# Kernel tuning notes

Hardware: AMD Instinct MI355X
Metric: run time of the kernel (lower is better)

The kernel has to match this reference:

```python
import jax, jax.numpy as jnp
import numpy as np

N = 10000      # nodes
E = 160000     # edges (before self-loops)
IN = 256
NEG_SLOPE = 0.2  # PyG GATConv default


def gat_layer(x, src, dst, W, a_src, a_dst, bias, heads, concat, n):
    # x: [n, in_dim]; W: [in_dim, heads*C]; a_src/a_dst: [heads, C]
    C = W.shape[1] // heads
    h = (x @ W).reshape(n, heads, C)                      # [n,H,C]
    es = jnp.einsum('nhc,hc->nh', h, a_src)               # [n,H]
    ed = jnp.einsum('nhc,hc->nh', h, a_dst)               # [n,H]
    e = jax.nn.leaky_relu(es[src] + ed[dst], NEG_SLOPE)   # [E,H]
    # segment softmax over destination node (every node has a self-loop)
    emax = jax.ops.segment_max(e, dst, num_segments=n)    # [n,H]
    al = jnp.exp(e - emax[dst])                           # [E,H]
    den = jax.ops.segment_sum(al, dst, num_segments=n)    # [n,H]
    al = al / den[dst]
    out = jax.ops.segment_sum(h[src] * al[:, :, None], dst, num_segments=n)  # [n,H,C]
    out = out.reshape(n, heads * C) if concat else out.mean(axis=1)
    return out + bias


def setup_inputs() -> dict:
    key = jax.random.key(0)
    ks = jax.random.split(key, 16)
    s = 0.05
    p = lambda k, shp: jax.random.normal(k, shp, dtype=jnp.float32) * s
    return {
        'x': jax.random.normal(ks[0], (N, IN), dtype=jnp.float32),
        'edge_index': jax.random.randint(ks[1], (2, E), 0, N, dtype=jnp.int64),
        'proj_w': p(ks[2], (IN, 512)), 'proj_b': jnp.zeros((512,), jnp.float32),
        'w1': p(ks[3], (512, 4 * 512)),  'as1': p(ks[4], (4, 512)), 'ad1': p(ks[5], (4, 512)),  'b1': jnp.zeros((2048,), jnp.float32),
        'w2': p(ks[6], (2048, 4 * 512)), 'as2': p(ks[7], (4, 512)), 'ad2': p(ks[8], (4, 512)),  'b2': jnp.zeros((2048,), jnp.float32),
        'w3': p(ks[9], (2048, 2 * 512)), 'as3': p(ks[10], (2, 512)), 'ad3': p(ks[11], (2, 512)), 'b3': jnp.zeros((512,), jnp.float32),
    }


def reference(x, edge_index, proj_w, proj_b, w1, as1, ad1, b1,
              w2, as2, ad2, b2, w3, as3, ad3, b3):
    n = x.shape[0]
    loops = jnp.arange(n, dtype=edge_index.dtype)
    src = jnp.concatenate([edge_index[0], loops])   # PyG add_self_loops=True
    dst = jnp.concatenate([edge_index[1], loops])
    h = x @ proj_w + proj_b                         # dropout is identity in eval
    h = gat_layer(h, src, dst, w1, as1, ad1, b1, 4, True, n)
    h = jax.nn.elu(h)
    h = gat_layer(h, src, dst, w2, as2, ad2, b2, 4, True, n)
    h = jax.nn.elu(h)
    h = gat_layer(h, src, dst, w3, as3, ad3, b3, 2, False, n)
    return h
```

## Files before the change

### kernel.cpp

```cpp
#include <hip/hip_runtime.h>
#include <hip/hip_bf16.h>
#include <math.h>

#define CDIV(a,b) (((a)+(b)-1)/(b))

typedef __bf16  bf16x8 __attribute__((ext_vector_type(8)));
typedef float   f32x4  __attribute__((ext_vector_type(4)));
typedef unsigned short u16x8 __attribute__((ext_vector_type(8)));
typedef unsigned short u16x4 __attribute__((ext_vector_type(4)));

__device__ __forceinline__ float bf2f(unsigned short u) {
    union { unsigned int i; float f; } x; x.i = ((unsigned int)u) << 16; return x.f;
}
__device__ __forceinline__ unsigned short f2bf(float f) {
    union { float f; unsigned int i; } x; x.f = f;
    unsigned int r = x.i + 0x7fff + ((x.i >> 16) & 1);
    return (unsigned short)(r >> 16);
}

__global__ void hist_kernel(const int* __restrict__ ei, int* __restrict__ deg,
                            int E, int Et) {
    int e = blockIdx.x * blockDim.x + threadIdx.x;
    if (e >= Et) return;
    int d = (e < E) ? ei[E + e] : (e - E);
    atomicAdd(&deg[d], 1);
}

__global__ void scan_kernel(const int* __restrict__ deg, int* __restrict__ off, int n) {
    __shared__ int wsum[16];
    __shared__ int carry_s;
    int t = threadIdx.x, lane = t & 63, wv = t >> 6;
    if (t == 0) carry_s = 0;
    __syncthreads();
    for (int base = 0; base < n; base += 1024) {
        int v = (base + t < n) ? deg[base + t] : 0;
        int x = v;
#pragma unroll
        for (int o = 1; o < 64; o <<= 1) {
            int y = __shfl_up(x, o);
            if (lane >= o) x += y;
        }
        if (lane == 63) wsum[wv] = x;
        __syncthreads();
        if (wv == 0 && lane < 16) {
            int s = wsum[lane];
#pragma unroll
            for (int o = 1; o < 16; o <<= 1) {
                int y = __shfl_up(s, o);
                if (lane >= o) s += y;
            }
            wsum[lane] = s;
        }
        __syncthreads();
        int wprev = (wv == 0) ? 0 : wsum[wv - 1];
        int incl = carry_s + wprev + x;
        if (base + t < n) off[base + t] = incl - v;
        __syncthreads();
        if (t == 1023) carry_s = incl;
        __syncthreads();
    }
    if (t == 0) off[n] = carry_s;
}

__global__ void scatter_kernel(const int* __restrict__ ei, const int* __restrict__ off,
                               int* __restrict__ cur, int* __restrict__ csr,
                               int E, int Et) {
    int e = blockIdx.x * blockDim.x + threadIdx.x;
    if (e >= Et) return;
    int s, d;
    if (e < E) { s = ei[e]; d = ei[E + e]; } else { s = e - E; d = s; }
    int pos = off[d] + atomicAdd(&cur[d], 1);
    csr[pos] = s;
}

__global__ void prep_t_kernel(const float* __restrict__ wa, __hip_bfloat16* __restrict__ wta,
                              const float* __restrict__ wb, __hip_bfloat16* __restrict__ wtb,
                              const float* __restrict__ wc, __hip_bfloat16* __restrict__ wtc,
                              int t0, int t1, int t2) {
    __shared__ float tile[32][33];
    int bid = blockIdx.x;
    const float* w; __hip_bfloat16* wt; int K, N, r;
    if (bid < t0)      { w = wa; wt = wta; K = 512;  N = 2048; r = bid; }
    else if (bid < t1) { w = wb; wt = wtb; K = 2048; N = 2048; r = bid - t0; }
    else               { w = wc; wt = wtc; K = 2048; N = 1024; r = bid - t1; }
    (void)t2;
    int kt = K >> 5;
    int kb = (r % kt) * 32, nb = (r / kt) * 32;
    int tx = threadIdx.x & 31, ty = threadIdx.x >> 5;
    for (int i = ty; i < 32; i += 8)
        tile[i][tx] = w[(size_t)(kb + i) * N + nb + tx];
    __syncthreads();
    for (int i = ty; i < 32; i += 8)
        wt[(size_t)(nb + i) * K + kb + tx] = __float2bfloat16(tile[tx][i]);
}

__global__ void cvt2_kernel(const float* __restrict__ a, __hip_bfloat16* __restrict__ ao,
                            int na4,
                            const float* __restrict__ b, __hip_bfloat16* __restrict__ bo,
                            int nb4) {
    int i = blockIdx.x * blockDim.x + threadIdx.x;
    const float* src; __hip_bfloat16* dst; int idx;
    if (i < na4) { src = a; dst = ao; idx = i * 4; }
    else if (i < na4 + nb4) { src = b; dst = bo; idx = (i - na4) * 4; }
    else return;
    float4 v = *(const float4*)(src + idx);
    dst[idx + 0] = __float2bfloat16(v.x);
    dst[idx + 1] = __float2bfloat16(v.y);
    dst[idx + 2] = __float2bfloat16(v.z);
    dst[idx + 3] = __float2bfloat16(v.w);
}

__global__ void beff_kernel(const float* __restrict__ pb, const float* __restrict__ w1,
                            float* __restrict__ beff, int N) {
    int j  = blockIdx.x * 256 + threadIdx.x;
    int k0 = blockIdx.y * 64;
    float s = 0.f;
#pragma unroll
    for (int k = 0; k < 64; k++)
        s = fmaf(pb[k0 + k], w1[(size_t)(k0 + k) * N + j], s);
    atomicAdd(&beff[j], s);
}

__global__ void va_kernel(const __hip_bfloat16* __restrict__ w_efft,
                          const float* __restrict__ b_eff,
                          const float* __restrict__ as1, const float* __restrict__ ad1,
                          const float* __restrict__ b1,
                          float* __restrict__ va, float* __restrict__ cvec,
                          float* __restrict__ b1s) {
    int j = blockIdx.x, t = threadIdx.x;
    if (j == 8) {
        for (int i = t; i < 2048; i += 256) b1s[i] = b_eff[i] + b1[i];
        return;
    }
    int h = j & 3;
    const float* a = ((j < 4) ? as1 : ad1) + h * 512;
    __shared__ float aLDS[512];
    __shared__ float red[256];
    for (int c = t; c < 512; c += 256) aLDS[c] = a[c];
    __syncthreads();
    float acc = 0.f;
    const unsigned short* wb = (const unsigned short*)w_efft + (size_t)h * 512 * 256 + t;
    for (int c = 0; c < 512; c++)
        acc = fmaf(aLDS[c], bf2f(wb[(size_t)c * 256]), acc);
    va[j * 256 + t] = acc;
    float cp = b_eff[h * 512 + t] * aLDS[t] + b_eff[h * 512 + 256 + t] * aLDS[256 + t];
    red[t] = cp;
    __syncthreads();
    for (int s = 128; s > 0; s >>= 1) {
        if (t < s) red[t] += red[t + s];
        __syncthreads();
    }
    if (t == 0) cvec[j] = red[0];
}

__global__ void es1_kernel(const __hip_bfloat16* __restrict__ x_bf,
                           const float* __restrict__ va, const float* __restrict__ cvec,
                           float* __restrict__ es, float* __restrict__ ed) {
    int node = blockIdx.x, l = threadIdx.x;
    u16x4 xv = *(const u16x4*)((const unsigned short*)x_bf + (size_t)node * 256 + l * 4);
    float xf[4];
#pragma unroll
    for (int k = 0; k < 4; k++) xf[k] = bf2f(xv[k]);
    float dot[8];
#pragma unroll
    for (int j = 0; j < 8; j++) {
        float4 v = *(const float4*)(va + j * 256 + l * 4);
        dot[j] = xf[0] * v.x + xf[1] * v.y + xf[2] * v.z + xf[3] * v.w;
    }
#pragma unroll
    for (int j = 0; j < 8; j++)
        for (int o = 32; o; o >>= 1) dot[j] += __shfl_down(dot[j], o);
    if (l == 0) {
#pragma unroll
        for (int h = 0; h < 4; h++) {
            es[node * 4 + h] = dot[h] + cvec[h];
            ed[node * 4 + h] = dot[4 + h] + cvec[4 + h];
        }
    }
}

__global__ __launch_bounds__(256) void agg1x_kernel(
    const __hip_bfloat16* __restrict__ x_bf, const float* __restrict__ es,
    const float* __restrict__ ed, const int* __restrict__ csr,
    const int* __restrict__ off, __hip_bfloat16* __restrict__ z)
{
    __shared__ float alds[64][4];
    __shared__ int   slds[64];
    int d = blockIdx.x, t = threadIdx.x;
    int beg = off[d], end = off[d + 1];
    float acc[4] = {0.f, 0.f, 0.f, 0.f}, den[4] = {0.f, 0.f, 0.f, 0.f};
    float edd[4];
#pragma unroll
    for (int h = 0; h < 4; h++) edd[h] = ed[d * 4 + h];
    const unsigned short* xb = (const unsigned short*)x_bf;

    for (int cb = beg; cb < end; cb += 64) {
        int cl = end - cb; if (cl > 64) cl = 64;
        int i = t >> 2, h = t & 3;
        if (i < cl) {
            int s = csr[cb + i];
            if (h == 0) slds[i] = s;
            float e = es[s * 4 + h] + edd[h];
            e = (e > 0.f) ? e : 0.2f * e;
            alds[i][h] = __expf(e);
        }
        __syncthreads();
        for (int ii = 0; ii < cl; ii++) {
            int s = slds[ii];
            float xv = bf2f(xb[(size_t)s * 256 + t]);
#pragma unroll
            for (int hh = 0; hh < 4; hh++) {
                float a = alds[ii][hh];
                den[hh] += a;
                acc[hh] = fmaf(a, xv, acc[hh]);
            }
        }
        __syncthreads();
    }
    unsigned short* zb = (unsigned short*)z + (size_t)d * 1024;
#pragma unroll
    for (int h = 0; h < 4; h++)
        zb[h * 256 + t] = f2bf(acc[h] / den[h]);
}

__device__ __forceinline__ void gload16(void* lds, const void* g) {
    __builtin_amdgcn_global_load_lds(
        (const __attribute__((address_space(1))) void*)g,
        (__attribute__((address_space(3))) void*)lds, 16, 0, 0);
}

__global__ __launch_bounds__(256) void gemm_bf16_kernel(
    const __hip_bfloat16* __restrict__ A,
    const __hip_bfloat16* __restrict__ BT,
    const float* __restrict__ bias,
    __hip_bfloat16* __restrict__ Cb,
    int M, int N, int K, int lda, int hko, int do_elu,
    int MB, int NB, int XT, int NBH)
{
    __shared__ __align__(16) __hip_bfloat16 As[128 * 32];
    __shared__ __align__(16) __hip_bfloat16 Bs[128 * 32];

    const int bid  = blockIdx.x;
    const int xcd  = bid & 7;
    const int slot = bid >> 3;
    const int per_yh = XT * NBH;
    const int yh    = slot / per_yh;
    const int rem   = slot - yh * per_yh;
    const int x_sub = rem / NBH;
    const int ys    = rem - x_sub * NBH;
    const int yb    = yh * NBH + ys;
    const int xb    = xcd * XT + x_sub;
    if (xb >= MB || yb >= NB) return;

    const int tid = threadIdx.x;
    const int m0 = xb * 128, n0 = yb * 128;
    const int w = tid >> 6, l = tid & 63;
    const int wm = (w & 1) * 64, wn = (w >> 1) * 64;
    const int lm = l & 15, lq = l >> 4;

    f32x4 acc[4][4] = {};

    const int arow = tid >> 2;
    const int acol = (tid & 3) * 8;
    const __hip_bfloat16* Ag = A + (size_t)(m0 + arow) * lda + acol + (n0 >> 9) * hko;
    const __hip_bfloat16* Bg = BT + (size_t)(n0 + arow) * K + acol;
    char* AsW = (char*)As + (w << 10);
    char* BsW = (char*)Bs + (w << 10);

    for (int k0 = 0; k0 < K; k0 += 32) {
        gload16(AsW,        Ag + k0);
        gload16(AsW + 4096, Ag + (size_t)64 * lda + k0);
        gload16(BsW,        Bg + k0);
        gload16(BsW + 4096, Bg + (size_t)64 * K + k0);
        __syncthreads();
        bf16x8 af[4], bfr[4];
#pragma unroll
        for (int i = 0; i < 4; i++)
            af[i] = *(const bf16x8*)(As + (wm + i * 16 + lm) * 32 + lq * 8);
#pragma unroll
        for (int j = 0; j < 4; j++)
            bfr[j] = *(const bf16x8*)(Bs + (wn + j * 16 + lm) * 32 + lq * 8);
#pragma unroll
        for (int i = 0; i < 4; i++)
#pragma unroll
            for (int j = 0; j < 4; j++)
                acc[i][j] = __builtin_amdgcn_mfma_f32_16x16x32_bf16(
                    af[i], bfr[j], acc[i][j], 0, 0, 0);
        __syncthreads();
    }

#pragma unroll
    for (int i = 0; i < 4; i++) {
        int rb = m0 + wm + i * 16 + lq * 4;
#pragma unroll
        for (int r = 0; r < 4; r++) {
            int row = rb + r;
            if (row >= M) continue;
#pragma unroll
            for (int j = 0; j < 4; j++) {
                int col = n0 + wn + j * 16 + lm;
                float v = acc[i][j][r];
                if (bias) v += bias[col];
                if (do_elu) v = (v > 0.f) ? v : expm1f(v);
                Cb[(size_t)row * N + col] = __float2bfloat16(v);
            }
        }
    }
}

__global__ __launch_bounds__(512, 2) void gemm256_kernel(
    const __hip_bfloat16* __restrict__ A,
    const __hip_bfloat16* __restrict__ BT,
    __hip_bfloat16* __restrict__ Cb,
    int M, int N, int K, int MT, int nfull)
{
    __shared__ __align__(16) char smem[131072];
    const int NT = K >> 6;

    const int cpx  = gridDim.x >> 3;
    const int bid  = blockIdx.x;
    const int slot = (bid & 7) * cpx + (bid >> 3);
    int mt, ntl;
    if (slot < nfull) { mt = slot % MT; ntl = slot / MT; }
    else              { ntl = nfull / MT; mt = (nfull % MT) + (slot - nfull); }
    const int m0 = mt << 8, n0 = ntl << 8;

    const int tid = threadIdx.x;
    const int w  = tid >> 6, l = tid & 63;
    const int wr = w >> 2, wc = w & 3;
    const int lm = l & 15, lq = l >> 4;

    const int srow = tid >> 3;
    const int scol = ((l & 7) << 3) ^ ((l >> 3) << 3);
    const __hip_bfloat16* As0 = A  + (size_t)(m0 + srow) * K + scol;
    const __hip_bfloat16* Bs0 = BT + (size_t)(n0 + srow) * K + scol;
    const size_t rs64  = (size_t)64  * K;
    const size_t rs128 = (size_t)128 * K;
    char* const stA = smem +          ((size_t)w << 10);
    char* const stB = smem + 65536 +  ((size_t)w << 10);

    auto STAGE_A = [&](int par, int hf, int tt) {
        char* d = stA + (((par << 1) | hf) << 14);
        const __hip_bfloat16* s = As0 + (size_t)hf * rs128 + (tt << 6);
        gload16(d,        s);
        gload16(d + 8192, s + rs64);
    };
    auto STAGE_B = [&](int par, int hf, int tt) {
        char* d = stB + (((par << 1) | hf) << 14);
        const __hip_bfloat16* s = Bs0 + (size_t)hf * rs128 + (tt << 6);
        gload16(d,        s);
        gload16(d + 8192, s + rs64);
    };

    const int roff = lm << 7;
    const int xm   = (lm & 7) << 4;
    const int off0 = (lq << 4) ^ xm;
    const int off1 = off0 ^ 64;
    const int bsel = 65536 + ((wc & 1) << 13);

    f32x4  acc[8][4] = {};
    bf16x8 af[8][2];
    bf16x8 bfr[2][2];

    STAGE_A(0, 0, 0); STAGE_A(0, 1, 0);
    STAGE_B(0, 0, 0); STAGE_B(0, 1, 0);
    STAGE_A(1, 0, 1); STAGE_A(1, 1, 1);
    asm volatile("s_waitcnt vmcnt(4)" ::: "memory");
    __builtin_amdgcn_s_barrier();

    for (int t = 0; t < NT; ++t) {
        const int par = t & 1;
        const char* aS = smem + (((par << 1) | wr)        << 14) + roff;
        const char* bS = smem + (((par << 1) | (wc >> 1)) << 14) + bsel + roff;

#pragma unroll
        for (int i = 0; i < 4; ++i) {
            af[i][0] = *(const bf16x8*)(aS + i * 2048 + off0);
            af[i][1] = *(const bf16x8*)(aS + i * 2048 + off1);
        }
#pragma unroll
        for (int j = 0; j < 2; ++j) {
            bfr[j][0] = *(const bf16x8*)(bS + j * 2048 + off0);
            bfr[j][1] = *(const bf16x8*)(bS + j * 2048 + off1);
        }
        if (t + 1 < NT) STAGE_B(par ^ 1, 0, t + 1);
        __builtin_amdgcn_s_barrier();
        asm volatile("s_waitcnt lgkmcnt(0)" ::: "memory");
        __builtin_amdgcn_sched_barrier(0);
        __builtin_amdgcn_s_setprio(1);
#pragma unroll
        for (int i = 0; i < 4; ++i)
#pragma unroll
            for (int j = 0; j < 2; ++j) {
                acc[i][j] = __builtin_amdgcn_mfma_f32_16x16x32_bf16(af[i][0], bfr[j][0], acc[i][j], 0, 0, 0);
                acc[i][j] = __builtin_amdgcn_mfma_f32_16x16x32_bf16(af[i][1], bfr[j][1], acc[i][j], 0, 0, 0);
            }
        __builtin_amdgcn_s_setprio(0);
        __builtin_amdgcn_s_barrier();

#pragma unroll
        for (int i = 4; i < 8; ++i) {
            af[i][0] = *(const bf16x8*)(aS + i * 2048 + off0);
            af[i][1] = *(const bf16x8*)(aS + i * 2048 + off1);
        }
        if (t + 1 < NT) STAGE_B(par ^ 1, 1, t + 1);
        __builtin_amdgcn_s_barrier();
        asm volatile("s_waitcnt lgkmcnt(0)" ::: "memory");
        __builtin_amdgcn_sched_barrier(0);
        __builtin_amdgcn_s_setprio(1);
#pragma unroll
        for (int i = 4; i < 8; ++i)
#pragma unroll
            for (int j = 0; j < 2; ++j) {
                acc[i][j] = __builtin_amdgcn_mfma_f32_16x16x32_bf16(af[i][0], bfr[j][0], acc[i][j], 0, 0, 0);
                acc[i][j] = __builtin_amdgcn_mfma_f32_16x16x32_bf16(af[i][1], bfr[j][1], acc[i][j], 0, 0, 0);
            }
        __builtin_amdgcn_s_setprio(0);
        __builtin_amdgcn_s_barrier();

#pragma unroll
        for (int j = 0; j < 2; ++j) {
            bfr[j][0] = *(const bf16x8*)(bS + (j + 2) * 2048 + off0);
            bfr[j][1] = *(const bf16x8*)(bS + (j + 2) * 2048 + off1);
        }
        if (t + 2 < NT) STAGE_A(par, 0, t + 2);
        __builtin_amdgcn_s_barrier();
        asm volatile("s_waitcnt lgkmcnt(0)" ::: "memory");
        __builtin_amdgcn_sched_barrier(0);
        __builtin_amdgcn_s_setprio(1);
#pragma unroll
        for (int i = 0; i < 4; ++i)
#pragma unroll
            for (int j = 0; j < 2; ++j) {
                acc[i][j + 2] = __builtin_amdgcn_mfma_f32_16x16x32_bf16(af[i][0], bfr[j][0], acc[i][j + 2], 0, 0, 0);
                acc[i][j + 2] = __builtin_amdgcn_mfma_f32_16x16x32_bf16(af[i][1], bfr[j][1], acc[i][j + 2], 0, 0, 0);
            }
        __builtin_amdgcn_s_setprio(0);
        __builtin_amdgcn_s_barrier();

        if (t + 2 < NT) STAGE_A(par, 1, t + 2);
        __builtin_amdgcn_s_barrier();
        __builtin_amdgcn_sched_barrier(0);
        __builtin_amdgcn_s_setprio(1);
#pragma unroll
        for (int i = 4; i < 8; ++i)
#pragma unroll
            for (int j = 0; j < 2; ++j) {
                acc[i][j + 2] = __builtin_amdgcn_mfma_f32_16x16x32_bf16(af[i][0], bfr[j][0], acc[i][j + 2], 0, 0, 0);
                acc[i][j + 2] = __builtin_amdgcn_mfma_f32_16x16x32_bf16(af[i][1], bfr[j][1], acc[i][j + 2], 0, 0, 0);
            }
        __builtin_amdgcn_s_setprio(0);
        if (t + 2 < NT)      { asm volatile("s_waitcnt vmcnt(4)" ::: "memory"); }
        else if (t + 1 < NT) { asm volatile("s_waitcnt vmcnt(0)" ::: "memory"); }
        __builtin_amdgcn_s_barrier();
    }

#pragma unroll
    for (int i = 0; i < 8; ++i) {
        int rb = m0 + wr * 128 + i * 16 + lq * 4;
#pragma unroll
        for (int r = 0; r < 4; ++r) {
            int row = rb + r;
            if (row >= M) continue;
#pragma unroll
            for (int j = 0; j < 4; ++j) {
                int col = n0 + wc * 64 + j * 16 + lm;
                Cb[(size_t)row * N + col] = __float2bfloat16(acc[i][j][r]);
            }
        }
    }
}

__global__ __launch_bounds__(256, 2) void gemm128_kernel(
    const __hip_bfloat16* __restrict__ A,
    const __hip_bfloat16* __restrict__ BT,
    __hip_bfloat16* __restrict__ Cb,
    int M, int N, int K, int mode, int RT)
{
    __shared__ __align__(16) char smem[65536];
    const int NT = K >> 6;

    const int cpx  = gridDim.x >> 3;
    const int bid  = blockIdx.x;
    const int slot = (bid & 7) * cpx + (bid >> 3);
    int r, c;
    if (mode == 0) { r = slot % RT; c = slot / RT; }
    else {
        if (slot < 96) { c = 12 + slot / 48; r = 32 + slot % 48; }
        else           { int u = slot - 96; c = 14 + u / 80; r = u % 80; }
    }
    const int m0 = r << 7, n0 = c << 7;

    const int tid = threadIdx.x;
    const int w = tid >> 6, l = tid & 63;
    const int wm = (w & 1) << 6, wn = (w >> 1) << 6;
    const int lm = l & 15, lq = l >> 4;

    const int srow = tid >> 3;
    const int scol = (((tid & 7) ^ ((tid >> 3) & 7)) << 3);
    const __hip_bfloat16* Ag = A  + (size_t)(m0 + srow) * K + scol;
    const __hip_bfloat16* Bg = BT + (size_t)(n0 + srow) * K + scol;
    const size_t rs32 = (size_t)32 * K;
    char* const dA = smem +         ((size_t)w << 10);
    char* const dB = smem + 16384 + ((size_t)w << 10);

    auto STAGE = [&](int par, int tt) {
        char* pa = dA + (par << 15);
        char* pb = dB + (par << 15);
        const __hip_bfloat16* sa = Ag + (tt << 6);
        const __hip_bfloat16* sb = Bg + (tt << 6);
#pragma unroll
        for (int s = 0; s < 4; ++s) {
            gload16(pa + (s << 12), sa + (size_t)s * rs32);
            gload16(pb + (s << 12), sb + (size_t)s * rs32);
        }
    };

    const int roff = lm << 7;
    const int off0 = (lq << 4) ^ ((lm & 7) << 4);
    const int off1 = off0 ^ 64;

    f32x4 acc[4][4] = {};

    STAGE(0, 0);
    asm volatile("s_waitcnt vmcnt(0)" ::: "memory");
    __builtin_amdgcn_s_barrier();

    for (int t = 0; t < NT; ++t) {
        const int par = t & 1;
        if (t + 1 < NT) STAGE(par ^ 1, t + 1);
        const char* aS = smem + (par << 15) +         wm * 128 + roff;
        const char* bS = smem + (par << 15) + 16384 + wn * 128 + roff;
        bf16x8 af[4][2], bfr[4][2];
#pragma unroll
        for (int i = 0; i < 4; ++i) {
            af[i][0]  = *(const bf16x8*)(aS + i * 2048 + off0);
            af[i][1]  = *(const bf16x8*)(aS + i * 2048 + off1);
            bfr[i][0] = *(const bf16x8*)(bS + i * 2048 + off0);
            bfr[i][1] = *(const bf16x8*)(bS + i * 2048 + off1);
        }
        asm volatile("s_waitcnt lgkmcnt(0)" ::: "memory");
        __builtin_amdgcn_sched_barrier(0);
        __builtin_amdgcn_s_setprio(1);
#pragma unroll
        for (int i = 0; i < 4; ++i)
#pragma unroll
            for (int j = 0; j < 4; ++j) {
                acc[i][j] = __builtin_amdgcn_mfma_f32_16x16x32_bf16(af[i][0], bfr[j][0], acc[i][j], 0, 0, 0);
                acc[i][j] = __builtin_amdgcn_mfma_f32_16x16x32_bf16(af[i][1], bfr[j][1], acc[i][j], 0, 0, 0);
            }
        __builtin_amdgcn_s_setprio(0);
        if (t + 1 < NT) asm volatile("s_waitcnt vmcnt(0)" ::: "memory");
        __builtin_amdgcn_s_barrier();
    }

#pragma unroll
    for (int i = 0; i < 4; ++i) {
        int rb = m0 + wm + i * 16 + lq * 4;
#pragma unroll
        for (int r2 = 0; r2 < 4; ++r2) {
            int row = rb + r2;
            if (row >= M) continue;
#pragma unroll
            for (int j = 0; j < 4; ++j) {
                int col = n0 + wn + j * 16 + lm;
                Cb[(size_t)row * N + col] = __float2bfloat16(acc[i][j][r2]);
            }
        }
    }
}

__global__ void esed_kernel(const __hip_bfloat16* __restrict__ h,
                            const float* __restrict__ a_src,
                            const float* __restrict__ a_dst,
                            float* __restrict__ es, float* __restrict__ ed, int H) {
    int nidx = blockIdx.x;
    int t = threadIdx.x;
    int head = t >> 6, lane = t & 63;
    const unsigned short* hp =
        (const unsigned short*)h + (size_t)nidx * H * 512 + head * 512 + lane * 8;
    const float* sp = a_src + head * 512 + lane * 8;
    const float* dp = a_dst + head * 512 + lane * 8;
    u16x8 hv = *(const u16x8*)hp;
    float4 s0 = *(const float4*)sp, s1 = *(const float4*)(sp + 4);
    float4 d0 = *(const float4*)dp, d1 = *(const float4*)(dp + 4);
    float hf[8];
#pragma unroll
    for (int k = 0; k < 8; k++) hf[k] = bf2f(hv[k]);
    float s = hf[0]*s0.x + hf[1]*s0.y + hf[2]*s0.z + hf[3]*s0.w
            + hf[4]*s1.x + hf[5]*s1.y + hf[6]*s1.z + hf[7]*s1.w;
    float d = hf[0]*d0.x + hf[1]*d0.y + hf[2]*d0.z + hf[3]*d0.w
            + hf[4]*d1.x + hf[5]*d1.y + hf[6]*d1.z + hf[7]*d1.w;
    for (int o = 32; o; o >>= 1) { s += __shfl_down(s, o); d += __shfl_down(d, o); }
    if (lane == 0) { es[nidx * H + head] = s; ed[nidx * H + head] = d; }
}

template<int H, int SHIFT>
__global__ __launch_bounds__(256) void alpharec_kernel(
    const float* __restrict__ es, const float* __restrict__ ed,
    const int* __restrict__ csr, const int* __restrict__ off,
    uint2* __restrict__ rec, int n)
{
    int d = blockIdx.x * 4 + (threadIdx.x >> 6);
    if (d >= n) return;
    int lane = threadIdx.x & 63;
    int beg = off[d], end = off[d + 1];
    float edd[H], den[H];
#pragma unroll
    for (int h = 0; h < H; h++) { edd[h] = ed[d * H + h]; den[h] = 0.f; }
    for (int i = beg + lane; i < end; i += 64) {
        int s = csr[i];
#pragma unroll
        for (int h = 0; h < H; h++) {
            float e = es[s * H + h] + edd[h];
            e = (e > 0.f) ? e : 0.2f * e;
            den[h] += __expf(e);
        }
    }
#pragma unroll
    for (int h = 0; h < H; h++) {
        for (int o = 32; o; o >>= 1) den[h] += __shfl_down(den[h], o);
        den[h] = __shfl(den[h], 0);
        den[h] = 1.f / den[h];
    }
    for (int i = beg + lane; i < end; i += 64) {
        int s = csr[i];
        unsigned obytes = ((unsigned)s) << SHIFT;
#pragma unroll
        for (int h = 0; h < H; h++) {
            float e = es[s * H + h] + edd[h];
            e = (e > 0.f) ? e : 0.2f * e;
            float a = __expf(e) * den[h];
            rec[(size_t)i * H + h] = make_uint2(obytes, __float_as_uint(a));
        }
    }
}

__global__ __launch_bounds__(256) void agg2s_kernel(
    const __hip_bfloat16* __restrict__ h, const uint2* __restrict__ rec,
    const int* __restrict__ off, const float* __restrict__ bias,
    __hip_bfloat16* __restrict__ outB, int n)
{
    const int bid   = blockIdx.x;
    const int slice = bid & 7;
    const int head  = slice >> 1;
    const int wvs   = (bid >> 3) * 4 + (threadIdx.x >> 6);
    const int lane  = threadIdx.x & 63;
    const int half  = lane >> 5;
    const int c0    = slice * 256 + (lane & 31) * 8;
    const unsigned c0b = (unsigned)c0 * 2;
    const char* hb = (const char*)h;
    float bv[8];
#pragma unroll
    for (int k = 0; k < 8; k++) bv[k] = bias[c0 + k];

    for (int d = wvs; d < n; d += 1024) {
        int beg = off[d], end = off[d + 1];
        float acc[8] = {0.f, 0.f, 0.f, 0.f, 0.f, 0.f, 0.f, 0.f};
        int i = beg + half;
        for (; i + 2 < end; i += 4) {
            uint2 r0 = rec[i * 4 + head];
            uint2 r1 = rec[(i + 2) * 4 + head];
            u16x8 v0 = *(const u16x8*)(hb + (size_t)(r0.x + c0b));
            u16x8 v1 = *(const u16x8*)(hb + (size_t)(r1.x + c0b));
            float a0 = __uint_as_float(r0.y);
            float a1 = __uint_as_float(r1.y);
#pragma unroll
            for (int k = 0; k < 8; k++) acc[k] = fmaf(a0, bf2f(v0[k]), acc[k]);
#pragma unroll
            for (int k = 0; k < 8; k++) acc[k] = fmaf(a1, bf2f(v1[k]), acc[k]);
        }
        for (; i < end; i += 2) {
            uint2 r0 = rec[i * 4 + head];
            u16x8 v0 = *(const u16x8*)(hb + (size_t)(r0.x + c0b));
            float a0 = __uint_as_float(r0.y);
#pragma unroll
            for (int k = 0; k < 8; k++) acc[k] = fmaf(a0, bf2f(v0[k]), acc[k]);
        }
#pragma unroll
        for (int k = 0; k < 8; k++) acc[k] += __shfl_xor(acc[k], 32);
        if (half == 0) {
            u16x8 ov;
#pragma unroll
            for (int k = 0; k < 8; k++) {
                float v = acc[k] + bv[k];
                v = (v > 0.f) ? v : expm1f(v);
                ov[k] = f2bf(v);
            }
            *(u16x8*)((unsigned short*)outB + (size_t)d * 2048 + c0) = ov;
        }
    }
}

__global__ __launch_bounds__(256) void agg3s_kernel(
    const __hip_bfloat16* __restrict__ h, const uint2* __restrict__ rec,
    const int* __restrict__ off, float* __restrict__ part, int n)
{
    const int bid   = blockIdx.x;
    const int xcd   = bid & 7;
    const int slice = xcd >> 1;
    const int head  = slice >> 1;
    const int sb    = ((bid >> 3) << 1) | (xcd & 1);
    const int wvs   = sb * 4 + (threadIdx.x >> 6);
    const int lane  = threadIdx.x & 63;
    const int half  = lane >> 5;
    const int c0    = slice * 256 + (lane & 31) * 8;
    const unsigned c0b = (unsigned)c0 * 2;
    const char* hb = (const char*)h;

    for (int d = wvs; d < n; d += 2048) {
        int beg = off[d], end = off[d + 1];
        float acc[8] = {0.f, 0.f, 0.f, 0.f, 0.f, 0.f, 0.f, 0.f};
        int i = beg + half;
        for (; i + 2 < end; i += 4) {
            uint2 r0 = rec[i * 2 + head];
            uint2 r1 = rec[(i + 2) * 2 + head];
            u16x8 v0 = *(const u16x8*)(hb + (size_t)(r0.x + c0b));
            u16x8 v1 = *(const u16x8*)(hb + (size_t)(r1.x + c0b));
            float a0 = __uint_as_float(r0.y);
            float a1 = __uint_as_float(r1.y);
#pragma unroll
            for (int k = 0; k < 8; k++) acc[k] = fmaf(a0, bf2f(v0[k]), acc[k]);
#pragma unroll
            for (int k = 0; k < 8; k++) acc[k] = fmaf(a1, bf2f(v1[k]), acc[k]);
        }
        for (; i < end; i += 2) {
            uint2 r0 = rec[i * 2 + head];
            u16x8 v0 = *(const u16x8*)(hb + (size_t)(r0.x + c0b));
            float a0 = __uint_as_float(r0.y);
#pragma unroll
            for (int k = 0; k < 8; k++) acc[k] = fmaf(a0, bf2f(v0[k]), acc[k]);
        }
#pragma unroll
        for (int k = 0; k < 8; k++) acc[k] += __shfl_xor(acc[k], 32);
        if (half == 0) {
            float* pp = part + (size_t)d * 1024 + c0;
            *(float4*)pp       = make_float4(acc[0], acc[1], acc[2], acc[3]);
            *(float4*)(pp + 4) = make_float4(acc[4], acc[5], acc[6], acc[7]);
        }
    }
}

__global__ void comb3_kernel(const float* __restrict__ part,
                             const float* __restrict__ b3,
                             float* __restrict__ out, int n) {
    int idx = blockIdx.x * 256 + threadIdx.x;
    if (idx >= n * 128) return;
    int d = idx >> 7, c = (idx & 127) * 4;
    float4 p0 = *(const float4*)(part + (size_t)d * 1024 + c);
    float4 p1 = *(const float4*)(part + (size_t)d * 1024 + 512 + c);
    float4 bb = *(const float4*)(b3 + c);
    float4 o;
    o.x = 0.5f * (p0.x + p1.x) + bb.x;
    o.y = 0.5f * (p0.y + p1.y) + bb.y;
    o.z = 0.5f * (p0.z + p1.z) + bb.z;
    o.w = 0.5f * (p0.w + p1.w) + bb.w;
    *(float4*)(out + (size_t)d * 512 + c) = o;
}

extern "C" void kernel_launch(void* const* d_in, const int* in_sizes, int n_in,
                              void* d_out, int out_size, void* d_ws, size_t ws_size,
                              hipStream_t stream) {
    const float* x      = (const float*)d_in[0];
    const int*   ei     = (const int*)  d_in[1];
    const float* proj_w = (const float*)d_in[2];
    const float* proj_b = (const float*)d_in[3];
    const float* w1  = (const float*)d_in[4];
    const float* as1 = (const float*)d_in[5];
    const float* ad1 = (const float*)d_in[6];
    const float* b1  = (const float*)d_in[7];
    const float* w2  = (const float*)d_in[8];
    const float* as2 = (const float*)d_in[9];
    const float* ad2 = (const float*)d_in[10];
    const float* b2  = (const float*)d_in[11];
    const float* w3  = (const float*)d_in[12];
    const float* as3 = (const float*)d_in[13];
    const float* ad3 = (const float*)d_in[14];
    const float* b3  = (const float*)d_in[15];

    const int n    = in_sizes[0] / 256;
    const int E    = in_sizes[1] / 2;
    const int Et   = E + n;
    const int MB   = CDIV(n, 128);
    const int MB2  = CDIV(n, 256);
    const int Mpad = MB2 * 256;
    const int XT   = CDIV(MB, 8);

    char* p = (char*)d_ws;
    auto carve = [&](size_t bytes) {
        void* r = (void*)p;
        p += (bytes + 255) & ~(size_t)255;
        return r;
    };
    __hip_bfloat16* h_bf    = (__hip_bfloat16*)carve((size_t)Mpad * 2048 * sizeof(__hip_bfloat16));
    __hip_bfloat16* act_bf  = (__hip_bfloat16*)carve((size_t)Mpad * 2048 * sizeof(__hip_bfloat16));
    __hip_bfloat16* x_bf    = (__hip_bfloat16*)carve((size_t)Mpad * 256 * sizeof(__hip_bfloat16));
    __hip_bfloat16* pw_bf   = (__hip_bfloat16*)carve((size_t)256 * 512 * sizeof(__hip_bfloat16));
    __hip_bfloat16* w1t     = (__hip_bfloat16*)carve((size_t)2048 * 512 * sizeof(__hip_bfloat16));
    __hip_bfloat16* w2t     = (__hip_bfloat16*)carve((size_t)2048 * 2048 * sizeof(__hip_bfloat16));
    __hip_bfloat16* w3t     = (__hip_bfloat16*)carve((size_t)1024 * 2048 * sizeof(__hip_bfloat16));
    __hip_bfloat16* w_efft  = (__hip_bfloat16*)carve((size_t)2048 * 256 * sizeof(__hip_bfloat16));
    float* b_eff = (float*)carve((size_t)2048 * sizeof(float));
    float* b1s   = (float*)carve((size_t)2048 * sizeof(float));
    float* va    = (float*)carve((size_t)8 * 256 * sizeof(float));
    float* cvec  = (float*)carve((size_t)8 * sizeof(float));
    float* es  = (float*)carve((size_t)n * 4 * sizeof(float));
    float* ed  = (float*)carve((size_t)n * 4 * sizeof(float));
    uint2* rec = (uint2*)carve((size_t)Et * 4 * sizeof(uint2));
    int* deg = (int*)carve((size_t)2 * n * sizeof(int));
    int* cur = deg + n;
    int* off = (int*)carve((size_t)(n + 1) * sizeof(int));
    int* csr = (int*)carve((size_t)Et * sizeof(int));
    __hip_bfloat16* z_bf = h_bf;
    float* part = (float*)act_bf;
    (void)ws_size; (void)n_in;

    hipMemsetAsync(deg, 0, 2 * n * sizeof(int), stream);
    hipMemsetAsync(b_eff, 0, 2048 * sizeof(float), stream);
    hist_kernel<<<CDIV(Et, 256), 256, 0, stream>>>(ei, deg, E, Et);
    scan_kernel<<<1, 1024, 0, stream>>>(deg, off, n);
    scatter_kernel<<<CDIV(Et, 256), 256, 0, stream>>>(ei, off, cur, csr, E, Et);

    const int t0 = (512 / 32) * (2048 / 32);
    const int t1 = t0 + (2048 / 32) * (2048 / 32);
    const int t2 = t1 + (2048 / 32) * (1024 / 32);
    prep_t_kernel<<<t2, 256, 0, stream>>>(w1, w1t, w2, w2t, w3, w3t, t0, t1, t2);
    const int na4 = 256 * 512 / 4, nb4 = n * 256 / 4;
    cvt2_kernel<<<CDIV(na4 + nb4, 256), 256, 0, stream>>>(proj_w, pw_bf, na4, x, x_bf, nb4);

    gemm_bf16_kernel<<<8 * 2 * 2, 256, 0, stream>>>(
        w1t, pw_bf, nullptr, w_efft, 2048, 256, 512, 512, 0, 0, 16, 2, 2, 2);
    beff_kernel<<<dim3(2048 / 256, 512 / 64), 256, 0, stream>>>(proj_b, w1, b_eff, 2048);

    va_kernel<<<9, 256, 0, stream>>>(w_efft, b_eff, as1, ad1, b1, va, cvec, b1s);

    es1_kernel<<<n, 64, 0, stream>>>(x_bf, va, cvec, es, ed);
    agg1x_kernel<<<n, 256, 0, stream>>>(x_bf, es, ed, csr, off, z_bf);
    gemm_bf16_kernel<<<8 * XT * 16, 256, 0, stream>>>(
        z_bf, w_efft, b1s, act_bf, n, 2048, 256, 1024, 256, 1, MB, 16, XT, 16);

    gemm256_kernel<<<256, 512, 0, stream>>>(act_bf, w2t, h_bf, n, 2048, 2048, 40, 240);
    gemm128_kernel<<<256, 256, 0, stream>>>(act_bf, w2t, h_bf, n, 2048, 2048, 1, 0);
    esed_kernel<<<n, 4 * 64, 0, stream>>>(h_bf, as2, ad2, es, ed, 4);
    alpharec_kernel<4, 12><<<CDIV(n, 4), 256, 0, stream>>>(es, ed, csr, off, rec, n);
    agg2s_kernel<<<2048, 256, 0, stream>>>(h_bf, rec, off, b2, act_bf, n);

    gemm128_kernel<<<640, 256, 0, stream>>>(act_bf, w3t, h_bf, n, 1024, 2048, 0, 80);
    esed_kernel<<<n, 2 * 64, 0, stream>>>(h_bf, as3, ad3, es, ed, 2);
    alpharec_kernel<2, 11><<<CDIV(n, 4), 256, 0, stream>>>(es, ed, csr, off, rec, n);
    agg3s_kernel<<<2048, 256, 0, stream>>>(h_bf, rec, off, part, n);
    comb3_kernel<<<CDIV(n * 128, 256), 256, 0, stream>>>(part, b3, (float*)d_out, n);
}
```

Before: 583.5 us.

## Split layer-1 aggregation into alpha precompute and vectorized gather; use 256-tile GEMM

```diff
diff --git a/kernel.cpp b/kernel.cpp
--- a/kernel.cpp
+++ b/kernel.cpp
@@ -179,48 +179,87 @@
     }
 }
 
-__global__ __launch_bounds__(256) void agg1x_kernel(
-    const __hip_bfloat16* __restrict__ x_bf, const float* __restrict__ es,
-    const float* __restrict__ ed, const int* __restrict__ csr,
-    const int* __restrict__ off, __hip_bfloat16* __restrict__ z)
+__global__ __launch_bounds__(256) void alpha4_kernel(
+    const float* __restrict__ es, const float* __restrict__ ed,
+    const int* __restrict__ csr, const int* __restrict__ off,
+    float4* __restrict__ al4, int n)
 {
-    __shared__ float alds[64][4];
-    __shared__ int   slds[64];
-    int d = blockIdx.x, t = threadIdx.x;
+    int d = blockIdx.x * 4 + (threadIdx.x >> 6);
+    if (d >= n) return;
+    int lane = threadIdx.x & 63;
     int beg = off[d], end = off[d + 1];
-    float acc[4] = {0.f, 0.f, 0.f, 0.f}, den[4] = {0.f, 0.f, 0.f, 0.f};
-    float edd[4];
-#pragma unroll
-    for (int h = 0; h < 4; h++) edd[h] = ed[d * 4 + h];
-    const unsigned short* xb = (const unsigned short*)x_bf;
-
-    for (int cb = beg; cb < end; cb += 64) {
-        int cl = end - cb; if (cl > 64) cl = 64;
-        int i = t >> 2, h = t & 3;
-        if (i < cl) {
-            int s = csr[cb + i];
-            if (h == 0) slds[i] = s;
+    float edd[4], den[4];
+#pragma unroll
+    for (int h = 0; h < 4; h++) { edd[h] = ed[d * 4 + h]; den[h] = 0.f; }
+    for (int i = beg + lane; i < end; i += 64) {
+        int s = csr[i];
+#pragma unroll
+        for (int h = 0; h < 4; h++) {
             float e = es[s * 4 + h] + edd[h];
             e = (e > 0.f) ? e : 0.2f * e;
-            alds[i][h] = __expf(e);
-        }
-        __syncthreads();
-        for (int ii = 0; ii < cl; ii++) {
-            int s = slds[ii];
-            float xv = bf2f(xb[(size_t)s * 256 + t]);
-#pragma unroll
-            for (int hh = 0; hh < 4; hh++) {
-                float a = alds[ii][hh];
-                den[hh] += a;
-                acc[hh] = fmaf(a, xv, acc[hh]);
-            }
-        }
-        __syncthreads();
-    }
+            den[h] += __expf(e);
+        }
+    }
+#pragma unroll
+    for (int h = 0; h < 4; h++) {
+        for (int o = 32; o; o >>= 1) den[h] += __shfl_down(den[h], o);
+        den[h] = __shfl(den[h], 0);
+        den[h] = 1.f / den[h];
+    }
+    for (int i = beg + lane; i < end; i += 64) {
+        int s = csr[i];
+        float a[4];
+#pragma unroll
+        for (int h = 0; h < 4; h++) {
+            float e = es[s * 4 + h] + edd[h];
+            e = (e > 0.f) ? e : 0.2f * e;
+            a[h] = __expf(e) * den[h];
+        }
+        al4[i] = make_float4(a[0], a[1], a[2], a[3]);
+    }
+}
+
+__global__ __launch_bounds__(256) void agg1x_kernel(
+    const __hip_bfloat16* __restrict__ x_bf, const float4* __restrict__ al4,
+    const int* __restrict__ csr, const int* __restrict__ off,
+    __hip_bfloat16* __restrict__ z)
+{
+    __shared__ float red[4][1024];
+    int d = blockIdx.x, t = threadIdx.x;
+    int w = t >> 6, l = t & 63;
+    int c0 = l * 4;
+    int beg = off[d], end = off[d + 1];
+    float acc[4][4] = {};
+    const unsigned short* xb = (const unsigned short*)x_bf;
+
+    for (int i = beg + w; i < end; i += 4) {
+        int s = csr[i];
+        float4 a = al4[i];
+        u16x4 xv = *(const u16x4*)(xb + (size_t)s * 256 + c0);
+        float xf[4];
+#pragma unroll
+        for (int k = 0; k < 4; k++) xf[k] = bf2f(xv[k]);
+#pragma unroll
+        for (int k = 0; k < 4; k++) {
+            acc[k][0] = fmaf(a.x, xf[k], acc[k][0]);
+            acc[k][1] = fmaf(a.y, xf[k], acc[k][1]);
+            acc[k][2] = fmaf(a.z, xf[k], acc[k][2]);
+            acc[k][3] = fmaf(a.w, xf[k], acc[k][3]);
+        }
+    }
+#pragma unroll
+    for (int h = 0; h < 4; h++)
+#pragma unroll
+        for (int k = 0; k < 4; k++)
+            red[w][h * 256 + c0 + k] = acc[k][h];
+    __syncthreads();
     unsigned short* zb = (unsigned short*)z + (size_t)d * 1024;
 #pragma unroll
-    for (int h = 0; h < 4; h++)
-        zb[h * 256 + t] = f2bf(acc[h] / den[h]);
+    for (int q = 0; q < 4; q++) {
+        int m = t + q * 256;
+        float v = red[0][m] + red[1][m] + red[2][m] + red[3][m];
+        zb[m] = f2bf(v);
+    }
 }
 
 __device__ __forceinline__ void gload16(void* lds, const void* g) {
@@ -311,8 +350,9 @@
 __global__ __launch_bounds__(512, 2) void gemm256_kernel(
     const __hip_bfloat16* __restrict__ A,
     const __hip_bfloat16* __restrict__ BT,
+    const float* __restrict__ bias,
     __hip_bfloat16* __restrict__ Cb,
-    int M, int N, int K, int MT, int nfull)
+    int M, int N, int K, int lda, int hko, int do_elu, int MT, int nfull)
 {
     __shared__ __align__(16) char smem[131072];
     const int NT = K >> 6;
@@ -332,24 +372,24 @@
 
     const int srow = tid >> 3;
     const int scol = ((l & 7) << 3) ^ ((l >> 3) << 3);
-    const __hip_bfloat16* As0 = A  + (size_t)(m0 + srow) * K + scol;
+    const __hip_bfloat16* As0 = A  + (size_t)(m0 + srow) * lda + scol + (n0 >> 9) * hko;
     const __hip_bfloat16* Bs0 = BT + (size_t)(n0 + srow) * K + scol;
-    const size_t rs64  = (size_t)64  * K;
-    const size_t rs128 = (size_t)128 * K;
+    const size_t rsA64 = (size_t)64 * lda, rsA128 = (size_t)128 * lda;
+    const size_t rsB64 = (size_t)64 * K,   rsB128 = (size_t)128 * K;
     char* const stA = smem +          ((size_t)w << 10);
     char* const stB = smem + 65536 +  ((size_t)w << 10);
 
     auto STAGE_A = [&](int par, int hf, int tt) {
         char* d = stA + (((par << 1) | hf) << 14);
-        const __hip_bfloat16* s = As0 + (size_t)hf * rs128 + (tt << 6);
+        const __hip_bfloat16* s = As0 + (size_t)hf * rsA128 + (tt << 6);
         gload16(d,        s);
-        gload16(d + 8192, s + rs64);
+        gload16(d + 8192, s + rsA64);
     };
     auto STAGE_B = [&](int par, int hf, int tt) {
         char* d = stB + (((par << 1) | hf) << 14);
-        const __hip_bfloat16* s = Bs0 + (size_t)hf * rs128 + (tt << 6);
+        const __hip_bfloat16* s = Bs0 + (size_t)hf * rsB128 + (tt << 6);
         gload16(d,        s);
-        gload16(d + 8192, s + rs64);
+        gload16(d + 8192, s + rsB64);
     };
 
     const int roff = lm << 7;
@@ -465,7 +505,10 @@
 #pragma unroll
             for (int j = 0; j < 4; ++j) {
                 int col = n0 + wc * 64 + j * 16 + lm;
-                Cb[(size_t)row * N + col] = __float2bfloat16(acc[i][j][r]);
+                float v = acc[i][j][r];
+                if (bias) v += bias[col];
+                if (do_elu) v = (v > 0.f) ? v : expm1f(v);
+                Cb[(size_t)row * N + col] = __float2bfloat16(v);
             }
         }
     }
@@ -781,10 +824,8 @@
     const int n    = in_sizes[0] / 256;
     const int E    = in_sizes[1] / 2;
     const int Et   = E + n;
-    const int MB   = CDIV(n, 128);
     const int MB2  = CDIV(n, 256);
     const int Mpad = MB2 * 256;
-    const int XT   = CDIV(MB, 8);
 
     char* p = (char*)d_ws;
     auto carve = [&](size_t bytes) {
@@ -813,6 +854,7 @@
     int* csr = (int*)carve((size_t)Et * sizeof(int));
     __hip_bfloat16* z_bf = h_bf;
     float* part = (float*)act_bf;
+    float4* al4 = (float4*)rec;
     (void)ws_size; (void)n_in;
 
     hipMemsetAsync(deg, 0, 2 * n * sizeof(int), stream);
@@ -835,11 +877,13 @@
     va_kernel<<<9, 256, 0, stream>>>(w_efft, b_eff, as1, ad1, b1, va, cvec, b1s);
 
     es1_kernel<<<n, 64, 0, stream>>>(x_bf, va, cvec, es, ed);
-    agg1x_kernel<<<n, 256, 0, stream>>>(x_bf, es, ed, csr, off, z_bf);
-    gemm_bf16_kernel<<<8 * XT * 16, 256, 0, stream>>>(
-        z_bf, w_efft, b1s, act_bf, n, 2048, 256, 1024, 256, 1, MB, 16, XT, 16);
-
-    gemm256_kernel<<<256, 512, 0, stream>>>(act_bf, w2t, h_bf, n, 2048, 2048, 40, 240);
+    alpha4_kernel<<<CDIV(n, 4), 256, 0, stream>>>(es, ed, csr, off, al4, n);
+    agg1x_kernel<<<n, 256, 0, stream>>>(x_bf, al4, csr, off, z_bf);
+    gemm256_kernel<<<320, 512, 0, stream>>>(
+        z_bf, w_efft, b1s, act_bf, n, 2048, 256, 1024, 256, 1, 40, 320);
+
+    gemm256_kernel<<<256, 512, 0, stream>>>(
+        act_bf, w2t, nullptr, h_bf, n, 2048, 2048, 2048, 0, 0, 40, 240);
     gemm128_kernel<<<256, 256, 0, stream>>>(act_bf, w2t, h_bf, n, 2048, 2048, 1, 0);
     esed_kernel<<<n, 4 * 64, 0, stream>>>(h_bf, as2, ad2, es, ed, 4);
     alpharec_kernel<4, 12><<<CDIV(n, 4), 256, 0, stream>>>(es, ed, csr, off, rec, n);
```

New measurement: 618.1 us. 5.9% more time.
